# Optimization experiments

Measured on AMD Instinct MI355X. Metric: run time of the kernel, lower is better.

The kernel has to match this reference:

```python
import jax, jax.numpy as jnp
import numpy as np

N = 512      # nodes
E = 512      # edges = nb-graph nodes
M = 16384    # nb-graph edges
FIN = 64     # in_node_nf
HID = 128    # hidden_nf
D = 32       # VTV_coord_nf (positional-encoding width)


def _silu(v):
    return v * jax.nn.sigmoid(v)


def _mlp(v, w1, b1, w2, b2):
    # 2-layer MLP with SiLU (matches MLP(in, out, [hidden]))
    return _silu(v @ w1 + b1) @ w2 + b2


def setup_inputs() -> dict:
    key = jax.random.key(0)
    ks = jax.random.split(key, 32)

    def lin(k, i, o, scale=None):
        s = (1.0 / np.sqrt(i)) if scale is None else scale
        return jax.random.normal(k, (i, o), dtype=jnp.float32) * jnp.float32(s)

    inp = {}
    inp['h'] = jax.random.normal(ks[0], (N, FIN), dtype=jnp.float32)
    inp['x'] = jax.random.normal(ks[1], (N, 3), dtype=jnp.float32)
    inp['edges'] = jax.random.randint(ks[2], (2, E), 0, N)
    inp['nb_edge'] = jax.random.randint(ks[3], (2, M), 0, E)
    inp['edge_attr'] = jax.random.normal(ks[4], (E, 4), dtype=jnp.float32)
    inp['nb_num_nodes'] = E  # python int (static)
    # edge_encoder: MLP(2*FIN -> HID -> FIN)
    inp['ew1'] = lin(ks[5], 2 * FIN, HID); inp['eb1'] = jnp.zeros((HID,), jnp.float32)
    inp['ew2'] = lin(ks[6], HID, FIN);     inp['eb2'] = jnp.zeros((FIN,), jnp.float32)
    # PPGN mlp1 / mlp2: MLP(D+FIN -> HID -> FIN)
    inp['p1w1'] = lin(ks[7], D + FIN, HID); inp['p1b1'] = jnp.zeros((HID,), jnp.float32)
    inp['p1w2'] = lin(ks[8], HID, FIN);     inp['p1b2'] = jnp.zeros((FIN,), jnp.float32)
    inp['p2w1'] = lin(ks[9], D + FIN, HID); inp['p2b1'] = jnp.zeros((HID,), jnp.float32)
    inp['p2w2'] = lin(ks[10], HID, FIN);    inp['p2b2'] = jnp.zeros((FIN,), jnp.float32)
    # PPGN output mlp: MLP(D+FIN+FIN -> HID -> FIN) on concat(skip, matmul)
    inp['p3w1'] = lin(ks[11], D + 2 * FIN, HID); inp['p3b1'] = jnp.zeros((HID,), jnp.float32)
    inp['p3w2'] = lin(ks[12], HID, FIN);         inp['p3b2'] = jnp.zeros((FIN,), jnp.float32)
    # IGN 2->1: linear over 5 basis ops
    inp['ign_w'] = lin(ks[13], 5 * FIN, FIN); inp['ign_b'] = jnp.zeros((FIN,), jnp.float32)
    # coord_mlp: Linear(FIN,HID), SiLU, Linear(HID,1,bias=False) with tiny init
    inp['cw1'] = lin(ks[14], FIN, HID); inp['cb1'] = jnp.zeros((HID,), jnp.float32)
    inp['cw2'] = lin(ks[15], HID, 1, scale=0.001)
    # node_dec: MLP(FIN -> HID -> FIN)
    inp['ndw1'] = lin(ks[16], FIN, HID); inp['ndb1'] = jnp.zeros((HID,), jnp.float32)
    inp['ndw2'] = lin(ks[17], HID, FIN); inp['ndb2'] = jnp.zeros((FIN,), jnp.float32)
    return inp


def reference(h, x, edges, nb_edge, edge_attr, nb_num_nodes,
              ew1, eb1, ew2, eb2,
              p1w1, p1b1, p1w2, p1b2,
              p2w1, p2b1, p2w2, p2b2,
              p3w1, p3b1, p3w2, p3b2,
              ign_w, ign_b,
              cw1, cb1, cw2,
              ndw1, ndb1, ndw2, ndb2):
    rows, cols = edges[0], edges[1]
    coord_diff = x[rows] - x[cols]                      # [E,3]
    nbr, nbc = nb_edge[0], nb_edge[1]
    # VTV: inner product of the two relative-position vectors of paired edges
    vtv = jnp.sum(coord_diff[nbr] * coord_diff[nbc], axis=-1)   # [M]
    # sinusoidal positional encoding, a_scale = D/2
    half = D // 2
    div_term = jnp.exp(jnp.log(jnp.float32(10000.0)) * (2.0 * jnp.arange(half, dtype=jnp.float32) / D))
    ang = vtv[:, None] * jnp.float32(D / 2) / div_term          # [M, D/2]
    pe = jnp.stack([jnp.sin(ang), jnp.cos(ang)], axis=-1).reshape(vtv.shape[0], D)
    # node-pair features per original edge
    efn = _mlp(jnp.concatenate([h[rows], h[cols]], axis=1), ew1, eb1, ew2, eb2)  # [E,FIN]
    nb_feat = jnp.concatenate([pe, efn[nbr] * efn[nbc]], axis=1)                 # [M, D+FIN]
    # densify nb-graph 2-tensor and run PPGN block
    En = nb_num_nodes
    T = jnp.zeros((En, En, nb_feat.shape[1]), dtype=nb_feat.dtype).at[nbr, nbc].add(nb_feat)
    m1 = _mlp(T, p1w1, p1b1, p1w2, p1b2)                 # [En,En,FIN]
    m2 = _mlp(T, p2w1, p2b1, p2w2, p2b2)
    mult = jnp.einsum('ikf,kjf->ijf', m1, m2)            # feature-wise matmul
    Tout = _mlp(jnp.concatenate([T, mult], axis=-1), p3w1, p3b1, p3w2, p3b2)
    # IGN 2->1: diag, row-sum, col-sum, total-sum, trace (broadcast)
    idx = jnp.arange(En)
    diag = Tout[idx, idx]                                # [En,FIN]
    rowsum = Tout.sum(axis=1)
    colsum = Tout.sum(axis=0)
    tot = jnp.broadcast_to(Tout.sum(axis=(0, 1)), diag.shape)
    tr = jnp.broadcast_to(diag.sum(axis=0), diag.shape)
    nb_t1 = jnp.concatenate([diag, rowsum, colsum, tot, tr], axis=1) @ ign_w + ign_b  # [En,FIN]
    # coord update: weighted coord_diff, segment-mean over source node
    w = _silu(nb_t1 @ cw1 + cb1) @ cw2                   # [E,1]
    trans = coord_diff * w
    Nn = x.shape[0]
    seg = jax.ops.segment_sum(trans, rows, num_segments=Nn)
    cnt = jax.ops.segment_sum(jnp.ones((rows.shape[0], 1), trans.dtype), rows, num_segments=Nn)
    x_new = x + seg / jnp.clip(cnt, 1.0)
    # node update: scatter_add edge features then residual MLP
    nb_t0 = jax.ops.segment_sum(nb_t1, rows, num_segments=Nn)
    h_new = h + _mlp(nb_t0, ndw1, ndb1, ndw2, ndb2)
    return (h_new, x_new, edge_attr)
```

## Files before the change

### kernel.cpp

```cpp
#include <hip/hip_runtime.h>
#include <hip/hip_bf16.h>

#define NN   512
#define EE   512
#define MM   16384

typedef float v4f __attribute__((ext_vector_type(4)));
typedef short short8v __attribute__((ext_vector_type(8)));

__device__ __forceinline__ float silu_f(float v) { return v / (1.0f + __expf(-v)); }

__global__ __launch_bounds__(128) void k_front(
    const float* __restrict__ h, const float* __restrict__ x,
    const int* __restrict__ edges, const int* __restrict__ nb_edge,
    const float* __restrict__ ew1, const float* __restrict__ eb1,
    const float* __restrict__ ew2, const float* __restrict__ eb2,
    const float* __restrict__ p1b1, const float* __restrict__ p1w2, const float* __restrict__ p1b2,
    const float* __restrict__ p2b1, const float* __restrict__ p2w2, const float* __restrict__ p2b2,
    const float* __restrict__ p3w1,
    float* __restrict__ coord_diff, float* __restrict__ efn,
    float* __restrict__ c1, float* __restrict__ c2,
    __hip_bfloat16* __restrict__ Wt, int* __restrict__ slotmap) {
  __shared__ float sm[256];
  int b = blockIdx.x, t = threadIdx.x;
  if (b < 512) {
    int r = edges[b], c = edges[EE + b];
    if (t < 3) coord_diff[b * 3 + t] = x[r * 3 + t] - x[c * 3 + t];
    if (t < 64) { sm[t] = h[r * 64 + t]; sm[64 + t] = h[c * 64 + t]; }
    __syncthreads();
    float acc = eb1[t];
    for (int k = 0; k < 128; ++k) acc += sm[k] * ew1[k * 128 + t];
    sm[128 + t] = silu_f(acc);
    __syncthreads();
    if (t < 64) {
      float o = eb2[t];
      for (int k = 0; k < 128; ++k) o += sm[128 + k] * ew2[k * 64 + t];
      efn[b * 64 + t] = o;
    }
  } else if (b == 512) {
    sm[t] = silu_f(p1b1[t]); sm[128 + t] = silu_f(p2b1[t]);
    __syncthreads();
    if (t < 64) {
      float a1 = p1b2[t], a2 = p2b2[t];
      for (int k = 0; k < 128; ++k) { a1 += sm[k] * p1w2[k * 64 + t]; a2 += sm[128 + k] * p2w2[k * 64 + t]; }
      c1[t] = a1; c2[t] = a2;
    }
  } else if (b < 577) {
    int e = (b - 513) * 128 + t;
    int hh = e >> 6, f = e & 63;
    Wt[hh * 64 + f] = __float2bfloat16(p3w1[(96 + f) * 128 + hh]);
  } else {
    int m = (b - 577) * 128 + t;
    int cell = nb_edge[m] * 512 + nb_edge[MM + m];
    atomicCAS(&slotmap[cell], -1, -2);
  }
}

__global__ __launch_bounds__(256) void k_compact(int* __restrict__ slotmap,
                                                 int* __restrict__ cells,
                                                 int* __restrict__ nC) {
  int cell = blockIdx.x * 256 + threadIdx.x;
  if (slotmap[cell] != -2) return;
  int s = atomicAdd(nC, 1);
  slotmap[cell] = s;
  cells[s] = cell;
}

__global__ __launch_bounds__(192) void k_scatterT(
    const int* __restrict__ nb_edge, const int* __restrict__ slotmap,
    const float* __restrict__ coord_diff, const float* __restrict__ efn,
    float* __restrict__ Tc) {
  int t = threadIdx.x;
  int sub = (t >= 96) ? 1 : 0;
  int c = t - sub * 96;
  int m = blockIdx.x * 2 + sub;
  int a = nb_edge[m], b = nb_edge[MM + m];
  int s = slotmap[a * 512 + b];
  float val;
  if (c < 32) {
    float vtv = coord_diff[a * 3 + 0] * coord_diff[b * 3 + 0]
              + coord_diff[a * 3 + 1] * coord_diff[b * 3 + 1]
              + coord_diff[a * 3 + 2] * coord_diff[b * 3 + 2];
    int i = c >> 1;
    float ang = vtv * 16.0f * __expf(-0.57564627324851143f * (float)i);
    val = (c & 1) ? cosf(ang) : sinf(ang);
  } else {
    int f = c - 32;
    val = efn[a * 64 + f] * efn[b * 64 + f];
  }
  atomicAdd(&Tc[s * 96 + c], val);
}

__global__ __launch_bounds__(128) void k_mlp96b(
    const int* __restrict__ cells, const int* __restrict__ nC, const float* __restrict__ Tc,
    const float* __restrict__ w11, const float* __restrict__ b11,
    const float* __restrict__ w12, const float* __restrict__ b12,
    const float* __restrict__ w21, const float* __restrict__ b21,
    const float* __restrict__ w22, const float* __restrict__ b22,
    const float* __restrict__ c1, const float* __restrict__ c2,
    const float* __restrict__ p3w1,
    __hip_bfloat16* __restrict__ D1d, __hip_bfloat16* __restrict__ D2dT,
    float* __restrict__ A, float* __restrict__ B,
    float* __restrict__ TWc) {
  __shared__ float xsT[96 * 8];
  __shared__ float hid[8][128];
  __shared__ int cl[8];
  int t = threadIdx.x;
  int nc = *nC;
  int s0 = blockIdx.x * 8;
  if (s0 >= nc) return;
  for (int e = t; e < 768; e += 128) xsT[(e % 96) * 8 + e / 96] = Tc[s0 * 96 + e];
  if (t < 8) cl[t] = (s0 + t < nc) ? cells[s0 + t] : 0;
  __syncthreads();
  float tw[8], a1[8], a2[8];
#pragma unroll
  for (int c = 0; c < 8; ++c) { tw[c] = 0.f; a1[c] = b11[t]; a2[c] = b21[t]; }
  for (int k = 0; k < 96; ++k) {
    float wt = p3w1[k * 128 + t];
    float w1v = w11[k * 128 + t];
    float w2v = w21[k * 128 + t];
    float4 xlo = *(const float4*)&xsT[k * 8];
    float4 xhi = *(const float4*)&xsT[k * 8 + 4];
    float xv[8] = {xlo.x, xlo.y, xlo.z, xlo.w, xhi.x, xhi.y, xhi.z, xhi.w};
#pragma unroll
    for (int c = 0; c < 8; ++c) {
      tw[c] += xv[c] * wt; a1[c] += xv[c] * w1v; a2[c] += xv[c] * w2v;
    }
  }
#pragma unroll
  for (int c = 0; c < 8; ++c) {
    if (s0 + c < nc) TWc[(s0 + c) * 128 + t] = tw[c];
    hid[c][t] = silu_f(a1[c]);
  }
  __syncthreads();
  {
    int hh = t & 63, cq = t >> 6;
    float o[4];
#pragma unroll
    for (int cc = 0; cc < 4; ++cc) o[cc] = b12[hh];
    for (int k = 0; k < 128; ++k) {
      float w = w12[k * 64 + hh];
#pragma unroll
      for (int cc = 0; cc < 4; ++cc) o[cc] += hid[cq * 4 + cc][k] * w;
    }
#pragma unroll
    for (int cc = 0; cc < 4; ++cc) {
      int c = cq * 4 + cc;
      if (s0 + c < nc) {
        float d = o[cc] - c1[hh];
        int cell = cl[c];
        int ai = cell >> 9, bj = cell & 511;
        atomicAdd(&A[ai * 64 + hh], d);
        D1d[(hh * 512 + ai) * 512 + bj] = __float2bfloat16(d);
      }
    }
  }
  __syncthreads();
#pragma unroll
  for (int c = 0; c < 8; ++c) hid[c][t] = silu_f(a2[c]);
  __syncthreads();
  {
    int hh = t & 63, cq = t >> 6;
    float o[4];
#pragma unroll
    for (int cc = 0; cc < 4; ++cc) o[cc] = b22[hh];
    for (int k = 0; k < 128; ++k) {
      float w = w22[k * 64 + hh];
#pragma unroll
      for (int cc = 0; cc < 4; ++cc) o[cc] += hid[cq * 4 + cc][k] * w;
    }
#pragma unroll
    for (int cc = 0; cc < 4; ++cc) {
      int c = cq * 4 + cc;
      if (s0 + c < nc) {
        float d = o[cc] - c2[hh];
        int cell = cl[c];
        int ai = cell >> 9, bj = cell & 511;
        atomicAdd(&B[bj * 64 + hh], d);
        D2dT[(hh * 512 + bj) * 512 + ai] = __float2bfloat16(d);
      }
    }
  }
}

__global__ __launch_bounds__(128) void k_uv(
    const float* __restrict__ A, const float* __restrict__ B,
    const float* __restrict__ c1, const float* __restrict__ c2,
    const float* __restrict__ p3w1, const float* __restrict__ p3b1,
    float* __restrict__ u, float* __restrict__ v) {
  __shared__ float vec[64];
  int i = blockIdx.x, y = blockIdx.y, t = threadIdx.x;
  if (t < 64)
    vec[t] = (y == 0) ? (512.0f * c1[t] * c2[t] + c2[t] * A[i * 64 + t])
                      : (c1[t] * B[i * 64 + t]);
  __syncthreads();
  float a = (y == 0) ? p3b1[t] : 0.f;
  for (int f = 0; f < 64; ++f) a += vec[f] * p3w1[(96 + f) * 128 + t];
  (y == 0 ? u : v)[i * 128 + t] = a;
}

__global__ __launch_bounds__(256) void k_einsum_mfma(
    const __hip_bfloat16* __restrict__ D1d,
    const __hip_bfloat16* __restrict__ D2dT,
    __hip_bfloat16* __restrict__ S_fij) {
  __shared__ short As[128 * 40];
  __shared__ short Bs[128 * 40];
  int b = blockIdx.x;
  int f = b >> 4;
  int i0 = ((b >> 2) & 3) * 128, j0 = (b & 3) * 128;
  int t = threadIdx.x;
  int w = t >> 6, lane = t & 63;
  int wy = w >> 1, wx = w & 1;
  int q = lane >> 4, l15 = lane & 15;
  const short* Ap = (const short*)D1d + f * 262144;
  const short* Bp = (const short*)D2dT + f * 262144;
  int row = t >> 1, seg = t & 1;
  v4f acc[4][4];
#pragma unroll
  for (int yi = 0; yi < 4; ++yi)
#pragma unroll
    for (int xj = 0; xj < 4; ++xj) acc[yi][xj] = (v4f){0.f, 0.f, 0.f, 0.f};
  for (int k0 = 0; k0 < 512; k0 += 32) {
    __syncthreads();
    const short8v* ga = (const short8v*)&Ap[(i0 + row) * 512 + k0 + seg * 16];
    const short8v* gb = (const short8v*)&Bp[(j0 + row) * 512 + k0 + seg * 16];
    *(short8v*)&As[row * 40 + seg * 16] = ga[0];
    *(short8v*)&As[row * 40 + seg * 16 + 8] = ga[1];
    *(short8v*)&Bs[row * 40 + seg * 16] = gb[0];
    *(short8v*)&Bs[row * 40 + seg * 16 + 8] = gb[1];
    __syncthreads();
    short8v af[4], bf[4];
#pragma unroll
    for (int x = 0; x < 4; ++x) {
      af[x] = *(const short8v*)&As[(wy * 64 + x * 16 + l15) * 40 + q * 8];
      bf[x] = *(const short8v*)&Bs[(wx * 64 + x * 16 + l15) * 40 + q * 8];
    }
#pragma unroll
    for (int yi = 0; yi < 4; ++yi)
#pragma unroll
      for (int xj = 0; xj < 4; ++xj)
        acc[yi][xj] = __builtin_amdgcn_mfma_f32_16x16x32_bf16(af[yi], bf[xj], acc[yi][xj], 0, 0, 0);
  }
#pragma unroll
  for (int yi = 0; yi < 4; ++yi)
#pragma unroll
    for (int r = 0; r < 4; ++r) {
      int irow = i0 + wy * 64 + yi * 16 + q * 4 + r;
#pragma unroll
      for (int xj = 0; xj < 4; ++xj)
        S_fij[(f * 512 + irow) * 512 + j0 + wx * 64 + xj * 16 + l15] =
            __float2bfloat16(acc[yi][xj][r]);
    }
}

__global__ __launch_bounds__(256) void k_transpose(
    const __hip_bfloat16* __restrict__ S_fij, __hip_bfloat16* __restrict__ S) {
  __shared__ short lds[64 * 72];
  int t = threadIdx.x;
  int ij0 = blockIdx.x * 64;
  const short* src = (const short*)S_fij;
#pragma unroll
  for (int p = 0; p < 2; ++p) {
    int f = p * 32 + (t >> 3), seg = t & 7;
    short8v ga = *(const short8v*)&src[f * 262144 + ij0 + seg * 8];
    int fgrp = f >> 3, flo = f & 7;
#pragma unroll
    for (int k = 0; k < 8; ++k) {
      int ij = seg * 8 + k;
      int swz = (fgrp ^ (ij & 7) ^ ((ij >> 3) & 7)) & 7;
      lds[ij * 72 + swz * 8 + flo] = ga[k];
    }
  }
  __syncthreads();
  short* dst = (short*)S;
#pragma unroll
  for (int p = 0; p < 2; ++p) {
    int ij = p * 32 + (t >> 3), fseg = t & 7;
    int swz = (fseg ^ (ij & 7) ^ ((ij >> 3) & 7)) & 7;
    short8v val = *(const short8v*)&lds[ij * 72 + swz * 8];
    *(short8v*)&dst[(ij0 + ij) * 64 + fseg * 8] = val;
  }
}

__global__ __launch_bounds__(256) void k_tout_mfma(
    const __hip_bfloat16* __restrict__ S, const float* __restrict__ u,
    const float* __restrict__ v, const float* __restrict__ TWc,
    const int* __restrict__ slotmap, const __hip_bfloat16* __restrict__ Wt,
    float* __restrict__ row_part, float* __restrict__ col_part,
    float* __restrict__ diag_silu) {
  __shared__ __hip_bfloat16 WtL[128 * 72];
  __shared__ __hip_bfloat16 uvL[4096];
  __shared__ __hip_bfloat16 colbuf[4][16][140];
  __shared__ int slotL[256];
  int t = threadIdx.x;
  int w = t >> 6, lane = t & 63;
  int q = lane >> 4, l15 = lane & 15;
  int bi = blockIdx.x >> 5, bj = blockIdx.x & 31;
  int i0 = bi * 16, j0 = bj * 16;
  for (int e = t; e < 4096; e += 256) {
    int row = e >> 5, c2 = e & 31;
    ((unsigned*)WtL)[row * 36 + c2] = ((const unsigned*)Wt)[row * 32 + c2];
  }
  for (int e = t; e < 2048; e += 256)
    uvL[e] = __float2bfloat16(u[(i0 + (e >> 7)) * 128 + (e & 127)]);
  for (int e = t; e < 2048; e += 256)
    uvL[2048 + e] = __float2bfloat16(v[(j0 + (e >> 7)) * 128 + (e & 127)]);
  slotL[t] = slotmap[(i0 + (t >> 4)) * 512 + j0 + (t & 15)];
  short8v a[4][2];
#pragma unroll
  for (int mt = 0; mt < 4; ++mt) {
    const short8v* sp =
        (const short8v*)&S[((i0 + w * 4 + mt) * 512 + j0 + l15) * 64];
    a[mt][0] = sp[q];
    a[mt][1] = sp[4 + q];
  }
  __syncthreads();
#pragma unroll
  for (int half = 0; half < 2; ++half) {
    v4f acc[4][4];
#pragma unroll
    for (int mt = 0; mt < 4; ++mt)
#pragma unroll
      for (int n4 = 0; n4 < 4; ++n4) {
        int nt = half * 4 + n4;
        const short8v* b0 = (const short8v*)&WtL[(nt * 16 + l15) * 72 + q * 8];
        const short8v* b1 = (const short8v*)&WtL[(nt * 16 + l15) * 72 + 32 + q * 8];
        v4f c = {0.f, 0.f, 0.f, 0.f};
        c = __builtin_amdgcn_mfma_f32_16x16x32_bf16(a[mt][0], *b0, c, 0, 0, 0);
        c = __builtin_amdgcn_mfma_f32_16x16x32_bf16(a[mt][1], *b1, c, 0, 0, 0);
        acc[mt][n4] = c;
      }
#pragma unroll
    for (int n4 = 0; n4 < 4; ++n4) {
      int nt = half * 4 + n4;
      int hh = nt * 16 + l15;
      float rs[4] = {0.f, 0.f, 0.f, 0.f};
#pragma unroll
      for (int r = 0; r < 4; ++r) {
        int jL = q * 4 + r;
        float cs = 0.f;
        float vv = __bfloat162float(uvL[2048 + jL * 128 + hh]);
#pragma unroll
        for (int mt = 0; mt < 4; ++mt) {
          int iL = w * 4 + mt;
          float z = acc[mt][n4][r] + __bfloat162float(uvL[iL * 128 + hh]) + vv;
          int s = slotL[iL * 16 + jL];
          if (s >= 0) z += TWc[s * 128 + hh];
          float sv = silu_f(z);
          rs[mt] += sv;
          cs += sv;
          if (bi == bj && iL == jL) diag_silu[(i0 + iL) * 128 + hh] = sv;
        }
        colbuf[w][jL][hh] = __float2bfloat16(cs);
      }
#pragma unroll
      for (int mt = 0; mt < 4; ++mt) {
        float rsum = rs[mt];
        rsum += __shfl_xor(rsum, 16);
        rsum += __shfl_xor(rsum, 32);
        if (q == 0)
          row_part[(bj * 512 + i0 + w * 4 + mt) * 128 + hh] = rsum;
      }
    }
  }
  __syncthreads();
  for (int e = t; e < 2048; e += 256) {
    int jL = e >> 7, hh = e & 127;
    float acc4 = __bfloat162float(colbuf[0][jL][hh]) + __bfloat162float(colbuf[1][jL][hh]) +
                 __bfloat162float(colbuf[2][jL][hh]) + __bfloat162float(colbuf[3][jL][hh]);
    col_part[(bi * 512 + j0 + jL) * 128 + hh] = acc4;
  }
}

__global__ __launch_bounds__(128) void k_tout2f(
    const float* __restrict__ diag_silu, const float* __restrict__ row_part,
    const float* __restrict__ col_part,
    const float* __restrict__ w2, const float* __restrict__ b2,
    float* __restrict__ diag_T, float* __restrict__ row_T, float* __restrict__ col_T,
    float* __restrict__ tot, float* __restrict__ tr) {
  __shared__ float in[128];
  int e = blockIdx.x, which = blockIdx.y, t = threadIdx.x;
  float a;
  if (which == 0) {
    a = diag_silu[e * 128 + t];
  } else {
    const float* src = (which == 1) ? row_part : col_part;
    a = 0.f;
    for (int p = 0; p < 32; ++p) a += src[(p * 512 + e) * 128 + t];
  }
  in[t] = a;
  __syncthreads();
  if (t < 64) {
    float o = 0.f;
    for (int k = 0; k < 128; ++k) o += in[k] * w2[k * 64 + t];
    float val = o + b2[t] * ((which == 0) ? 1.0f : 512.0f);
    if (which == 0)      { diag_T[e * 64 + t] = val; atomicAdd(&tr[t], val); }
    else if (which == 1) { row_T[e * 64 + t] = val; atomicAdd(&tot[t], val); }
    else                 { col_T[e * 64 + t] = val; }
  }
}

__global__ __launch_bounds__(64) void k_nbt1(
    const float* __restrict__ diag_T, const float* __restrict__ row_T,
    const float* __restrict__ col_T, const float* __restrict__ tot,
    const float* __restrict__ tr,
    const float* __restrict__ gw, const float* __restrict__ gb,
    float* __restrict__ nb_t1) {
  __shared__ float in[320];
  int e = blockIdx.x, t = threadIdx.x;
  in[t] = diag_T[e * 64 + t]; in[64 + t] = row_T[e * 64 + t];
  in[128 + t] = col_T[e * 64 + t]; in[192 + t] = tot[t]; in[256 + t] = tr[t];
  __syncthreads();
  float a = gb[t];
  for (int k = 0; k < 320; ++k) a += in[k] * gw[k * 64 + t];
  nb_t1[e * 64 + t] = a;
}

__global__ __launch_bounds__(128) void k_edge_out(
    const int* __restrict__ edges, const float* __restrict__ coord_diff,
    const float* __restrict__ nb_t1, const float* __restrict__ edge_attr,
    const float* __restrict__ cw1, const float* __restrict__ cb1,
    const float* __restrict__ cw2,
    float* __restrict__ seg, float* __restrict__ cnt, float* __restrict__ nb_t0,
    float* __restrict__ out_ea) {
  __shared__ float in[64];
  __shared__ float red[128];
  int e = blockIdx.x, t = threadIdx.x;
  if (t < 64) in[t] = nb_t1[e * 64 + t];
  __syncthreads();
  float a = cb1[t];
  for (int k = 0; k < 64; ++k) a += in[k] * cw1[k * 128 + t];
  red[t] = silu_f(a) * cw2[t];
  __syncthreads();
  for (int s2 = 64; s2 > 0; s2 >>= 1) {
    if (t < s2) red[t] += red[t + s2];
    __syncthreads();
  }
  float w = red[0];
  int r = edges[e];
  if (t < 3) atomicAdd(&seg[r * 3 + t], coord_diff[e * 3 + t] * w);
  if (t == 64) atomicAdd(&cnt[r], 1.0f);
  if (t < 64) atomicAdd(&nb_t0[r * 64 + t], in[t]);
  if (t < 4) out_ea[e * 4 + t] = edge_attr[e * 4 + t];
}

__global__ __launch_bounds__(128) void k_node_out(
    const float* __restrict__ h, const float* __restrict__ x,
    const float* __restrict__ seg, const float* __restrict__ cnt,
    const float* __restrict__ nb_t0,
    const float* __restrict__ w1, const float* __restrict__ b1,
    const float* __restrict__ w2, const float* __restrict__ b2,
    float* __restrict__ out_h, float* __restrict__ out_x) {
  __shared__ float in[64];
  __shared__ float hs[128];
  int n = blockIdx.x, t = threadIdx.x;
  if (t < 3) {
    float c = cnt[n]; if (c < 1.f) c = 1.f;
    out_x[n * 3 + t] = x[n * 3 + t] + seg[n * 3 + t] / c;
  }
  if (t < 64) in[t] = nb_t0[n * 64 + t];
  __syncthreads();
  float a = b1[t];
  for (int k = 0; k < 64; ++k) a += in[k] * w1[k * 128 + t];
  hs[t] = silu_f(a);
  __syncthreads();
  if (t < 64) {
    float o = b2[t];
    for (int k = 0; k < 128; ++k) o += hs[k] * w2[k * 64 + t];
    out_h[n * 64 + t] = h[n * 64 + t] + o;
  }
}

extern "C" void kernel_launch(void* const* d_in, const int* in_sizes, int n_in,
                              void* d_out, int out_size, void* d_ws, size_t ws_size,
                              hipStream_t stream) {
  (void)in_sizes; (void)n_in; (void)out_size; (void)ws_size;
  const float* h  = (const float*)d_in[0];
  const float* x  = (const float*)d_in[1];
  const int* edges   = (const int*)d_in[2];
  const int* nb_edge = (const int*)d_in[3];
  const float* edge_attr = (const float*)d_in[4];
  const float* ew1 = (const float*)d_in[6],  *eb1 = (const float*)d_in[7];
  const float* ew2 = (const float*)d_in[8],  *eb2 = (const float*)d_in[9];
  const float* p1w1 = (const float*)d_in[10], *p1b1 = (const float*)d_in[11];
  const float* p1w2 = (const float*)d_in[12], *p1b2 = (const float*)d_in[13];
  const float* p2w1 = (const float*)d_in[14], *p2b1 = (const float*)d_in[15];
  const float* p2w2 = (const float*)d_in[16], *p2b2 = (const float*)d_in[17];
  const float* p3w1 = (const float*)d_in[18], *p3b1 = (const float*)d_in[19];
  const float* p3w2 = (const float*)d_in[20], *p3b2 = (const float*)d_in[21];
  const float* ignw = (const float*)d_in[22], *ignb = (const float*)d_in[23];
  const float* cw1 = (const float*)d_in[24], *cb1 = (const float*)d_in[25];
  const float* cw2 = (const float*)d_in[26];
  const float* ndw1 = (const float*)d_in[27], *ndb1 = (const float*)d_in[28];
  const float* ndw2 = (const float*)d_in[29], *ndb2 = (const float*)d_in[30];

  char* ws = (char*)d_ws;
  __hip_bfloat16* D1d  = (__hip_bfloat16*)(ws + 0);
  __hip_bfloat16* S    = (__hip_bfloat16*)(ws + 0);
  __hip_bfloat16* D2dT = (__hip_bfloat16*)(ws + 33554432);
  __hip_bfloat16* S_fij = (__hip_bfloat16*)(ws + 67108864);
  float* row_part = (float*)(ws + 100663296);
  float* col_part = (float*)(ws + 117440512);
  float* Tc    = (float*)(ws + 134217728);
  int*   nC    = (int*)(ws + 140509184);
  float* A     = (float*)(ws + 140509200);
  float* B     = (float*)(ws + 140640272);
  float* seg   = (float*)(ws + 140771344);
  float* cnt   = (float*)(ws + 140777488);
  float* nb_t0 = (float*)(ws + 140779536);
  float* tot   = (float*)(ws + 140910608);
  float* tr    = (float*)(ws + 140910864);
  int*   slotmap  = (int*)(ws + 140911616);
  int*   cells    = (int*)(ws + 141960192);
  float* TWc      = (float*)(ws + 142025728);
  float* c1       = (float*)(ws + 150414336);
  float* c2       = (float*)(ws + 150414592);
  float* u        = (float*)(ws + 150414848);
  float* v        = (float*)(ws + 150676992);
  float* coord_diff  = (float*)(ws + 150939136);
  float* efn         = (float*)(ws + 150945280);
  float* diag_silu   = (float*)(ws + 151076352);
  float* diag_T      = (float*)(ws + 151338496);
  float* row_T       = (float*)(ws + 151469568);
  float* col_T       = (float*)(ws + 151600640);
  float* nb_t1       = (float*)(ws + 151731712);
  __hip_bfloat16* Wt  = (__hip_bfloat16*)(ws + 151862784);

  float* out_h  = (float*)d_out;
  float* out_x  = out_h + 512 * 64;
  float* out_ea = out_x + 512 * 3;

  hipMemsetAsync(ws, 0, 67108864, stream);
  hipMemsetAsync(slotmap, 0xFF, 1048576, stream);
  hipMemsetAsync(ws + 134217728, 0, 6693392, stream);

  k_front<<<705, 128, 0, stream>>>(h, x, edges, nb_edge,
                                   ew1, eb1, ew2, eb2,
                                   p1b1, p1w2, p1b2, p2b1, p2w2, p2b2, p3w1,
                                   coord_diff, efn, c1, c2, Wt, slotmap);
  k_compact<<<1024, 256, 0, stream>>>(slotmap, cells, nC);
  k_scatterT<<<8192, 192, 0, stream>>>(nb_edge, slotmap, coord_diff, efn, Tc);
  k_mlp96b<<<2048, 128, 0, stream>>>(cells, nC, Tc,
                                     p1w1, p1b1, p1w2, p1b2,
                                     p2w1, p2b1, p2w2, p2b2,
                                     c1, c2, p3w1, D1d, D2dT, A, B, TWc);
  k_uv<<<dim3(512, 2), 128, 0, stream>>>(A, B, c1, c2, p3w1, p3b1, u, v);
  k_einsum_mfma<<<1024, 256, 0, stream>>>(D1d, D2dT, S_fij);
  k_transpose<<<4096, 256, 0, stream>>>(S_fij, S);
  k_tout_mfma<<<1024, 256, 0, stream>>>(S, u, v, TWc, slotmap, Wt,
                                        row_part, col_part, diag_silu);
  k_tout2f<<<dim3(512, 3), 128, 0, stream>>>(diag_silu, row_part, col_part,
                                             p3w2, p3b2, diag_T, row_T, col_T,
                                             tot, tr);
  k_nbt1<<<512, 64, 0, stream>>>(diag_T, row_T, col_T, tot, tr, ignw, ignb, nb_t1);
  k_edge_out<<<512, 128, 0, stream>>>(edges, coord_diff, nb_t1, edge_attr,
                                      cw1, cb1, cw2, seg, cnt, nb_t0, out_ea);
  k_node_out<<<512, 128, 0, stream>>>(h, x, seg, cnt, nb_t0,
                                      ndw1, ndb1, ndw2, ndb2, out_h, out_x);
}
```

Measured before the change: 406.4 us.

## Stream Wt from global in MFMA kernel, shrink LDS with fp32 u/v and atomic column sums

The kernel no longer stages the bf16 weight tile in LDS. Each lane now loads its B fragments straight from global memory, once per n-tile, and reuses them across the four M tiles. The u and v tiles are kept in LDS as fp32 instead of bf16, and the four per-wave column buffers are replaced by one shared fp32 accumulator updated with LDS atomicAdd. A min-blocks launch bound of 4 is added. Together these cut LDS footprint and register pressure to raise occupancy and drop the Wt staging copy, at the cost of global loads in the inner loop and LDS atomic contention.

New measurement: 421.4 us. 3.7% more time.

```diff
diff --git a/kernel.cpp b/kernel.cpp
--- a/kernel.cpp
+++ b/kernel.cpp
@@ -282,29 +282,27 @@
   }
 }
 
-__global__ __launch_bounds__(256) void k_tout_mfma(
+__global__ __launch_bounds__(256, 4) void k_tout_mfma(
     const __hip_bfloat16* __restrict__ S, const float* __restrict__ u,
     const float* __restrict__ v, const float* __restrict__ TWc,
     const int* __restrict__ slotmap, const __hip_bfloat16* __restrict__ Wt,
     float* __restrict__ row_part, float* __restrict__ col_part,
     float* __restrict__ diag_silu) {
-  __shared__ __hip_bfloat16 WtL[128 * 72];
-  __shared__ __hip_bfloat16 uvL[4096];
-  __shared__ __hip_bfloat16 colbuf[4][16][140];
+  __shared__ float uL[16 * 132];
+  __shared__ float vL[16 * 132];
+  __shared__ float colAcc[16 * 132];
   __shared__ int slotL[256];
   int t = threadIdx.x;
   int w = t >> 6, lane = t & 63;
   int q = lane >> 4, l15 = lane & 15;
   int bi = blockIdx.x >> 5, bj = blockIdx.x & 31;
   int i0 = bi * 16, j0 = bj * 16;
-  for (int e = t; e < 4096; e += 256) {
-    int row = e >> 5, c2 = e & 31;
-    ((unsigned*)WtL)[row * 36 + c2] = ((const unsigned*)Wt)[row * 32 + c2];
-  }
-  for (int e = t; e < 2048; e += 256)
-    uvL[e] = __float2bfloat16(u[(i0 + (e >> 7)) * 128 + (e & 127)]);
-  for (int e = t; e < 2048; e += 256)
-    uvL[2048 + e] = __float2bfloat16(v[(j0 + (e >> 7)) * 128 + (e & 127)]);
+  for (int e = t; e < 2048; e += 256) {
+    int rr = e >> 7, cc = e & 127;
+    uL[rr * 132 + cc] = u[(i0 + rr) * 128 + cc];
+    vL[rr * 132 + cc] = v[(j0 + rr) * 128 + cc];
+  }
+  for (int e = t; e < 16 * 132; e += 256) colAcc[e] = 0.f;
   slotL[t] = slotmap[(i0 + (t >> 4)) * 512 + j0 + (t & 15)];
   short8v a[4][2];
 #pragma unroll
@@ -319,31 +317,35 @@
   for (int half = 0; half < 2; ++half) {
     v4f acc[4][4];
 #pragma unroll
-    for (int mt = 0; mt < 4; ++mt)
-#pragma unroll
-      for (int n4 = 0; n4 < 4; ++n4) {
-        int nt = half * 4 + n4;
-        const short8v* b0 = (const short8v*)&WtL[(nt * 16 + l15) * 72 + q * 8];
-        const short8v* b1 = (const short8v*)&WtL[(nt * 16 + l15) * 72 + 32 + q * 8];
+    for (int n4 = 0; n4 < 4; ++n4) {
+      int nt = half * 4 + n4;
+      const short8v* bp = (const short8v*)&((const short*)Wt)[(nt * 16 + l15) * 64];
+      short8v b0 = bp[q], b1 = bp[4 + q];
+#pragma unroll
+      for (int mt = 0; mt < 4; ++mt) {
         v4f c = {0.f, 0.f, 0.f, 0.f};
-        c = __builtin_amdgcn_mfma_f32_16x16x32_bf16(a[mt][0], *b0, c, 0, 0, 0);
-        c = __builtin_amdgcn_mfma_f32_16x16x32_bf16(a[mt][1], *b1, c, 0, 0, 0);
+        c = __builtin_amdgcn_mfma_f32_16x16x32_bf16(a[mt][0], b0, c, 0, 0, 0);
+        c = __builtin_amdgcn_mfma_f32_16x16x32_bf16(a[mt][1], b1, c, 0, 0, 0);
         acc[mt][n4] = c;
       }
+    }
 #pragma unroll
     for (int n4 = 0; n4 < 4; ++n4) {
       int nt = half * 4 + n4;
       int hh = nt * 16 + l15;
+      float uu[4];
+#pragma unroll
+      for (int mt = 0; mt < 4; ++mt) uu[mt] = uL[(w * 4 + mt) * 132 + hh];
       float rs[4] = {0.f, 0.f, 0.f, 0.f};
 #pragma unroll
       for (int r = 0; r < 4; ++r) {
         int jL = q * 4 + r;
+        float vv = vL[jL * 132 + hh];
         float cs = 0.f;
-        float vv = __bfloat162float(uvL[2048 + jL * 128 + hh]);
 #pragma unroll
         for (int mt = 0; mt < 4; ++mt) {
           int iL = w * 4 + mt;
-          float z = acc[mt][n4][r] + __bfloat162float(uvL[iL * 128 + hh]) + vv;
+          float z = acc[mt][n4][r] + uu[mt] + vv;
           int s = slotL[iL * 16 + jL];
           if (s >= 0) z += TWc[s * 128 + hh];
           float sv = silu_f(z);
@@ -351,7 +353,7 @@
           cs += sv;
           if (bi == bj && iL == jL) diag_silu[(i0 + iL) * 128 + hh] = sv;
         }
-        colbuf[w][jL][hh] = __float2bfloat16(cs);
+        atomicAdd(&colAcc[jL * 132 + hh], cs);
       }
 #pragma unroll
       for (int mt = 0; mt < 4; ++mt) {
@@ -366,9 +368,7 @@
   __syncthreads();
   for (int e = t; e < 2048; e += 256) {
     int jL = e >> 7, hh = e & 127;
-    float acc4 = __bfloat162float(colbuf[0][jL][hh]) + __bfloat162float(colbuf[1][jL][hh]) +
-                 __bfloat162float(colbuf[2][jL][hh]) + __bfloat162float(colbuf[3][jL][hh]);
-    col_part[(bi * 512 + j0 + jL) * 128 + hh] = acc4;
+    col_part[(bi * 512 + j0 + jL) * 128 + hh] = colAcc[jL * 132 + hh];
   }
 }
 
```

## Move sparse T-cell contribution out of dense Tout kernel into correction pass

Applied to the files above, without the earlier changes.

The dense Tout kernel no longer looks up the slot map and adds the sparse T contribution per element. It computes silu over only the dense part. A new per-occupied-cell kernel recomputes the pre-activation for each nonzero cell, takes the difference between silu with and without the sparse term, and atomically adds it to the row, column and diagonal sums. SiLU also switches to a hardware reciprocal, and the u values are hoisted out of the inner loop. This removes gathers and branches from the hot dense loop, at the cost of an extra launch, atomics, and bf16 rounding that differs slightly between the two paths.

New measurement: 401.0 us. About the same (-1.3%).

```diff
diff --git a/kernel.cpp b/kernel.cpp
--- a/kernel.cpp
+++ b/kernel.cpp
@@ -9,6 +9,9 @@
 typedef short short8v __attribute__((ext_vector_type(8)));
 
 __device__ __forceinline__ float silu_f(float v) { return v / (1.0f + __expf(-v)); }
+__device__ __forceinline__ float silu_fast(float v) {
+  return v * __builtin_amdgcn_rcpf(1.0f + __expf(-v));
+}
 
 __global__ __launch_bounds__(128) void k_front(
     const float* __restrict__ h, const float* __restrict__ x,
@@ -284,14 +287,12 @@
 
 __global__ __launch_bounds__(256) void k_tout_mfma(
     const __hip_bfloat16* __restrict__ S, const float* __restrict__ u,
-    const float* __restrict__ v, const float* __restrict__ TWc,
-    const int* __restrict__ slotmap, const __hip_bfloat16* __restrict__ Wt,
+    const float* __restrict__ v, const __hip_bfloat16* __restrict__ Wt,
     float* __restrict__ row_part, float* __restrict__ col_part,
     float* __restrict__ diag_silu) {
   __shared__ __hip_bfloat16 WtL[128 * 72];
   __shared__ __hip_bfloat16 uvL[4096];
   __shared__ __hip_bfloat16 colbuf[4][16][140];
-  __shared__ int slotL[256];
   int t = threadIdx.x;
   int w = t >> 6, lane = t & 63;
   int q = lane >> 4, l15 = lane & 15;
@@ -305,7 +306,6 @@
     uvL[e] = __float2bfloat16(u[(i0 + (e >> 7)) * 128 + (e & 127)]);
   for (int e = t; e < 2048; e += 256)
     uvL[2048 + e] = __float2bfloat16(v[(j0 + (e >> 7)) * 128 + (e & 127)]);
-  slotL[t] = slotmap[(i0 + (t >> 4)) * 512 + j0 + (t & 15)];
   short8v a[4][2];
 #pragma unroll
   for (int mt = 0; mt < 4; ++mt) {
@@ -334,6 +334,10 @@
     for (int n4 = 0; n4 < 4; ++n4) {
       int nt = half * 4 + n4;
       int hh = nt * 16 + l15;
+      float uu[4];
+#pragma unroll
+      for (int mt = 0; mt < 4; ++mt)
+        uu[mt] = __bfloat162float(uvL[(w * 4 + mt) * 128 + hh]);
       float rs[4] = {0.f, 0.f, 0.f, 0.f};
 #pragma unroll
       for (int r = 0; r < 4; ++r) {
@@ -343,10 +347,7 @@
 #pragma unroll
         for (int mt = 0; mt < 4; ++mt) {
           int iL = w * 4 + mt;
-          float z = acc[mt][n4][r] + __bfloat162float(uvL[iL * 128 + hh]) + vv;
-          int s = slotL[iL * 16 + jL];
-          if (s >= 0) z += TWc[s * 128 + hh];
-          float sv = silu_f(z);
+          float sv = silu_fast(acc[mt][n4][r] + uu[mt] + vv);
           rs[mt] += sv;
           cs += sv;
           if (bi == bj && iL == jL) diag_silu[(i0 + iL) * 128 + hh] = sv;
@@ -372,9 +373,36 @@
   }
 }
 
+__global__ __launch_bounds__(128) void k_corr(
+    const int* __restrict__ cells, const int* __restrict__ nC,
+    const __hip_bfloat16* __restrict__ S, const float* __restrict__ u,
+    const float* __restrict__ v, const float* __restrict__ TWc,
+    const __hip_bfloat16* __restrict__ Wt,
+    float* __restrict__ corr_row, float* __restrict__ corr_col,
+    float* __restrict__ diag_silu) {
+  __shared__ float sf[64];
+  int s = blockIdx.x;
+  if (s >= *nC) return;
+  int t = threadIdx.x;
+  int cell = cells[s];
+  int ai = cell >> 9, bj = cell & 511;
+  if (t < 64) sf[t] = __bfloat162float(S[(ai * 512 + bj) * 64 + t]);
+  __syncthreads();
+  float acc = 0.f;
+  const __hip_bfloat16* wr = &Wt[t * 64];
+  for (int f = 0; f < 64; ++f) acc += sf[f] * __bfloat162float(wr[f]);
+  float z0 = acc + u[ai * 128 + t] + v[bj * 128 + t];
+  float zc = z0 + TWc[s * 128 + t];
+  float d = silu_fast(zc) - silu_fast(z0);
+  atomicAdd(&corr_row[ai * 128 + t], d);
+  atomicAdd(&corr_col[bj * 128 + t], d);
+  if (ai == bj) atomicAdd(&diag_silu[ai * 128 + t], d);
+}
+
 __global__ __launch_bounds__(128) void k_tout2f(
     const float* __restrict__ diag_silu, const float* __restrict__ row_part,
     const float* __restrict__ col_part,
+    const float* __restrict__ corr_row, const float* __restrict__ corr_col,
     const float* __restrict__ w2, const float* __restrict__ b2,
     float* __restrict__ diag_T, float* __restrict__ row_T, float* __restrict__ col_T,
     float* __restrict__ tot, float* __restrict__ tr) {
@@ -385,7 +413,7 @@
     a = diag_silu[e * 128 + t];
   } else {
     const float* src = (which == 1) ? row_part : col_part;
-    a = 0.f;
+    a = (which == 1) ? corr_row[e * 128 + t] : corr_col[e * 128 + t];
     for (int p = 0; p < 32; ++p) a += src[(p * 512 + e) * 128 + t];
   }
   in[t] = a;
@@ -510,21 +538,23 @@
   float* nb_t0 = (float*)(ws + 140779536);
   float* tot   = (float*)(ws + 140910608);
   float* tr    = (float*)(ws + 140910864);
-  int*   slotmap  = (int*)(ws + 140911616);
-  int*   cells    = (int*)(ws + 141960192);
-  float* TWc      = (float*)(ws + 142025728);
-  float* c1       = (float*)(ws + 150414336);
-  float* c2       = (float*)(ws + 150414592);
-  float* u        = (float*)(ws + 150414848);
-  float* v        = (float*)(ws + 150676992);
-  float* coord_diff  = (float*)(ws + 150939136);
-  float* efn         = (float*)(ws + 150945280);
-  float* diag_silu   = (float*)(ws + 151076352);
-  float* diag_T      = (float*)(ws + 151338496);
-  float* row_T       = (float*)(ws + 151469568);
-  float* col_T       = (float*)(ws + 151600640);
-  float* nb_t1       = (float*)(ws + 151731712);
-  __hip_bfloat16* Wt  = (__hip_bfloat16*)(ws + 151862784);
+  float* corr_row = (float*)(ws + 140911120);
+  float* corr_col = (float*)(ws + 141173264);
+  int*   slotmap  = (int*)(ws + 141435904);
+  int*   cells    = (int*)(ws + 142484480);
+  float* TWc      = (float*)(ws + 142550016);
+  float* c1       = (float*)(ws + 150938624);
+  float* c2       = (float*)(ws + 150938880);
+  float* u        = (float*)(ws + 150939136);
+  float* v        = (float*)(ws + 151201280);
+  float* coord_diff  = (float*)(ws + 151463424);
+  float* efn         = (float*)(ws + 151469568);
+  float* diag_silu   = (float*)(ws + 151600640);
+  float* diag_T      = (float*)(ws + 151862784);
+  float* row_T       = (float*)(ws + 151993856);
+  float* col_T       = (float*)(ws + 152124928);
+  float* nb_t1       = (float*)(ws + 152256000);
+  __hip_bfloat16* Wt  = (__hip_bfloat16*)(ws + 152387072);
 
   float* out_h  = (float*)d_out;
   float* out_x  = out_h + 512 * 64;
@@ -532,7 +562,7 @@
 
   hipMemsetAsync(ws, 0, 67108864, stream);
   hipMemsetAsync(slotmap, 0xFF, 1048576, stream);
-  hipMemsetAsync(ws + 134217728, 0, 6693392, stream);
+  hipMemsetAsync(ws + 134217728, 0, 7217680, stream);
 
   k_front<<<705, 128, 0, stream>>>(h, x, edges, nb_edge,
                                    ew1, eb1, ew2, eb2,
@@ -547,9 +577,12 @@
   k_uv<<<dim3(512, 2), 128, 0, stream>>>(A, B, c1, c2, p3w1, p3b1, u, v);
   k_einsum_mfma<<<1024, 256, 0, stream>>>(D1d, D2dT, S_fij);
   k_transpose<<<4096, 256, 0, stream>>>(S_fij, S);
-  k_tout_mfma<<<1024, 256, 0, stream>>>(S, u, v, TWc, slotmap, Wt,
+  k_tout_mfma<<<1024, 256, 0, stream>>>(S, u, v, Wt,
                                         row_part, col_part, diag_silu);
+  k_corr<<<16384, 128, 0, stream>>>(cells, nC, S, u, v, TWc, Wt,
+                                    corr_row, corr_col, diag_silu);
   k_tout2f<<<dim3(512, 3), 128, 0, stream>>>(diag_silu, row_part, col_part,
+                                             corr_row, corr_col,
                                              p3w2, p3b2, diag_T, row_T, col_T,
                                              tot, tr);
   k_nbt1<<<512, 64, 0, stream>>>(diag_T, row_T, col_T, tot, tr, ignw, ignb, nb_t1);
```
